# Kernel optimization log

Measured on AMD Instinct MI355X. Metric: run time of the kernel, lower is better.

## Reference

```python
import jax, jax.numpy as jnp
import numpy as np

D = 1024
M = 16
H = D // M  # 64
EPS = 1e-05


def setup_inputs() -> dict:
    key = jax.random.key(0)
    ks = jax.random.split(key, 5)
    B, T = 4, 1024
    x = jax.random.normal(ks[0], (B, T, D), dtype=jnp.float32)
    norm_w = jnp.ones((D,), dtype=jnp.float32)
    s = 1.0 / np.sqrt(D)
    W_v = jax.random.uniform(ks[1], (D, D), dtype=jnp.float32, minval=-s, maxval=s)
    W_a = jax.random.uniform(ks[2], (H * M * (M + 1), D), dtype=jnp.float32, minval=-s, maxval=s)
    W_out = jax.random.uniform(ks[3], (D, D), dtype=jnp.float32, minval=-s, maxval=s)
    return {"x": x, "norm_w": norm_w, "W_v": W_v, "W_a": W_a, "W_out": W_out}


def _rmsnorm(x, w, eps=EPS):
    var = jnp.mean(jnp.square(x), axis=-1, keepdims=True)
    return x * jax.lax.rsqrt(var + eps) * w


def reference(x, norm_w, W_v, W_a, W_out):
    B, T, _ = x.shape
    h = _rmsnorm(x, norm_w)                              # [B,T,D]
    v = (h @ W_v.T).reshape(B, T, H, M)                  # [B,T,H,m]
    gate_logits = (h @ W_a.T).reshape(B, T, H, M, M + 1)
    gates = jax.nn.softmax(gate_logits, axis=-1)
    a0 = gates[..., 0]                                   # [B,T,H,m]
    A = gates[..., 1:]                                   # [B,T,H,m,m]

    # time-major for scan
    A_t = jnp.moveaxis(A, 1, 0)                          # [T,B,H,m,m]
    u_t = jnp.moveaxis(a0 * v, 1, 0)                     # [T,B,H,m]

    def step(state, inp):
        At, ut = inp
        new = jnp.einsum('bhij,bhj->bhi', At, state) + ut
        return new, new

    init = jnp.zeros((B, H, M), dtype=x.dtype)
    _, ys = jax.lax.scan(step, init, (A_t, u_t))         # ys: [T,B,H,m]
    h_out = jnp.moveaxis(ys, 0, 1).reshape(B, T, D)
    return x + h_out @ W_out.T
```

## Files before the change

kernel.cpp:

```cpp
#include <hip/hip_runtime.h>
#include <hip/hip_bf16.h>
#include <math.h>

#define B_DIM 4
#define T_DIM 1024
#define D_DIM 1024
#define M_DIM 16
#define H_DIM 64
#define NT    4096
#define NA    17408
#define NCAT  18432
#define EPSV  1e-5f
#define CL    16
#define NC    64

typedef __bf16 bf16_t;
typedef __bf16 bf16x4 __attribute__((ext_vector_type(4)));
typedef __bf16 bf16x8 __attribute__((ext_vector_type(8)));
typedef float  f32x4  __attribute__((ext_vector_type(4)));

#define PBAR() do { asm volatile("" ::: "memory"); __builtin_amdgcn_s_barrier(); asm volatile("" ::: "memory"); } while (0)

__global__ __launch_bounds__(256) void prep_kernel(const float* __restrict__ x,
                                                   const float* __restrict__ nw,
                                                   const float* __restrict__ Wa,
                                                   const float* __restrict__ Wv,
                                                   const float* __restrict__ Wo,
                                                   bf16_t* __restrict__ h,
                                                   bf16_t* __restrict__ wcat,
                                                   bf16_t* __restrict__ wo) {
  int tid = threadIdx.x;
  if (blockIdx.x < NT) {
    int row = blockIdx.x;
    const float4* xr = reinterpret_cast<const float4*>(x + (size_t)row * D_DIM);
    float4 xv = xr[tid];
    float ss = xv.x * xv.x + xv.y * xv.y + xv.z * xv.z + xv.w * xv.w;
#pragma unroll
    for (int m = 1; m < 64; m <<= 1) ss += __shfl_xor(ss, m, 64);
    __shared__ float red[4];
    int lane = tid & 63, wid = tid >> 6;
    if (lane == 0) red[wid] = ss;
    __syncthreads();
    float tot = red[0] + red[1] + red[2] + red[3];
    float scale = rsqrtf(tot * (1.0f / D_DIM) + EPSV);
    float4 wv = reinterpret_cast<const float4*>(nw)[tid];
    bf16x4 o;
    o[0] = (bf16_t)(xv.x * scale * wv.x);
    o[1] = (bf16_t)(xv.y * scale * wv.y);
    o[2] = (bf16_t)(xv.z * scale * wv.z);
    o[3] = (bf16_t)(xv.w * scale * wv.w);
    reinterpret_cast<bf16x4*>(h)[(size_t)row * 256 + tid] = o;
  } else {
    constexpr int NA4 = NA * D_DIM / 4;
    constexpr int NV4 = D_DIM * D_DIM / 4;
    constexpr int total = NA4 + 2 * NV4;
    int nb = gridDim.x - NT;
    int idx = (blockIdx.x - NT) * 256 + tid;
    int stride = nb * 256;
    for (; idx < total; idx += stride) {
      const float* src; bf16_t* dst; int j;
      if (idx < NA4)            { src = Wa; dst = wcat; j = idx; }
      else if (idx < NA4 + NV4) { src = Wv; dst = wcat + (size_t)NA * D_DIM; j = idx - NA4; }
      else                      { src = Wo; dst = wo; j = idx - NA4 - NV4; }
      float4 v = reinterpret_cast<const float4*>(src)[j];
      bf16x4 o;
      o[0] = (bf16_t)v.x; o[1] = (bf16_t)v.y; o[2] = (bf16_t)v.z; o[3] = (bf16_t)v.w;
      reinterpret_cast<bf16x4*>(dst)[j] = o;
    }
  }
}

__global__ __launch_bounds__(256) void gemm_out_kernel(const bf16_t* __restrict__ A,
                                                       const bf16_t* __restrict__ Bw,
                                                       float* __restrict__ Cout,
                                                       const float* __restrict__ resid,
                                                       int Ndim, int K) {
  constexpr int BM = 128, BN = 128, BK = 32;
  __shared__ bf16_t As[BM * BK];
  __shared__ bf16_t Bs[BN * BK];

  int tid = threadIdx.x;
  int lane = tid & 63;
  int wid = tid >> 6;
  int wm = wid >> 1, wn = wid & 1;
  int bm = blockIdx.x * BM;
  int bn = blockIdx.y * BN;
  int l15 = lane & 15;
  int l4 = lane >> 4;

  f32x4 acc[4][4];
#pragma unroll
  for (int i = 0; i < 4; i++)
#pragma unroll
    for (int j = 0; j < 4; j++) acc[i][j] = (f32x4){0.f, 0.f, 0.f, 0.f};

  const bf16_t* Ag = A + (size_t)bm * K;
  const bf16_t* Bg = Bw + (size_t)bn * K;
  int srow_lane = lane >> 2;
  int scol = (lane & 3) * 8;

  for (int k0 = 0; k0 < K; k0 += BK) {
#pragma unroll
    for (int i = 0; i < 2; i++) {
      int rbase = wid * 32 + i * 16;
      int r = rbase + srow_lane;
      __builtin_amdgcn_global_load_lds(
          (const __attribute__((address_space(1))) void*)(Ag + (size_t)r * K + k0 + scol),
          (__attribute__((address_space(3))) void*)(As + rbase * BK), 16, 0, 0);
      __builtin_amdgcn_global_load_lds(
          (const __attribute__((address_space(1))) void*)(Bg + (size_t)r * K + k0 + scol),
          (__attribute__((address_space(3))) void*)(Bs + rbase * BK), 16, 0, 0);
    }
    __syncthreads();

    const bf16x8* Asv = reinterpret_cast<const bf16x8*>(As);
    const bf16x8* Bsv = reinterpret_cast<const bf16x8*>(Bs);
    bf16x8 af[4], bfr[4];
#pragma unroll
    for (int mf = 0; mf < 4; mf++)
      af[mf] = Asv[(wm * 64 + mf * 16 + l15) * 4 + l4];
#pragma unroll
    for (int nf = 0; nf < 4; nf++)
      bfr[nf] = Bsv[(wn * 64 + nf * 16 + l15) * 4 + l4];
#pragma unroll
    for (int mf = 0; mf < 4; mf++)
#pragma unroll
      for (int nf = 0; nf < 4; nf++)
        acc[mf][nf] = __builtin_amdgcn_mfma_f32_16x16x32_bf16(af[mf], bfr[nf], acc[mf][nf], 0, 0, 0);
    __syncthreads();
  }

#pragma unroll
  for (int mf = 0; mf < 4; mf++)
#pragma unroll
    for (int nf = 0; nf < 4; nf++)
#pragma unroll
      for (int i = 0; i < 4; i++) {
        int row = bm + wm * 64 + mf * 16 + l4 * 4 + i;
        int col = bn + wn * 64 + nf * 16 + l15;
        size_t idx = (size_t)row * Ndim + col;
        Cout[idx] = acc[mf][nf][i] + resid[idx];
      }
}

__global__ __launch_bounds__(512, 2) void gemm256_nt_kernel(const bf16_t* __restrict__ A,
                                                            const bf16_t* __restrict__ Bw,
                                                            bf16_t* __restrict__ Clg,
                                                            float* __restrict__ Cv) {
  constexpr int K = 1024;
  constexpr int G = K / 64;
  __shared__ bf16_t As[2 * 16384];
  __shared__ bf16_t Bs[2 * 16384];

  const int tid = threadIdx.x;
  const int lane = tid & 63;
  const int w = tid >> 6;
  const int wm = w >> 2;
  const int wn = w & 3;
  const int l15 = lane & 15;
  const int l4 = lane >> 4;

  const int bm = blockIdx.x * 256;
  const int bn = blockIdx.y * 256;

  const bf16_t* Ag = A + (size_t)bm * K;
  const bf16_t* Bg = Bw + (size_t)bn * K;

  int growi[2], gcoli[2];
#pragma unroll
  for (int j = 0; j < 2; ++j) {
    int E = j * 4096 + tid * 8;
    int sub = E >> 9, e = E & 511;
    int rin = e >> 5, cs = e & 31;
    int cin = cs ^ ((rin & 8) ? 16 : 0);
    growi[j] = (sub >> 1) * 16 + rin;
    gcoli[j] = (sub & 1) * 32 + cin;
  }

  const int fbase = l15 * 32 + ((l4 * 8) ^ ((l15 & 8) ? 16 : 0));

  f32x4 acc[8][4];
#pragma unroll
  for (int i = 0; i < 8; i++)
#pragma unroll
    for (int j = 0; j < 4; j++) acc[i][j] = (f32x4){0.f, 0.f, 0.f, 0.f};

  bf16x8 ALo[8], AHi[8], B0r[4], B1r[4];

  auto stageHalf = [&](const bf16_t* Gp, bf16_t* Lp, int bufp, int half, int t2) {
#pragma unroll
    for (int j = 0; j < 2; ++j) {
      const bf16_t* src = Gp + (size_t)(half * 128 + growi[j]) * K + t2 * 64 + gcoli[j];
      __builtin_amdgcn_global_load_lds(
          (const __attribute__((address_space(1))) void*)src,
          (__attribute__((address_space(3))) void*)(Lp + bufp * 16384 + half * 8192 + j * 4096 + w * 512),
          16, 0, 0);
    }
  };

  auto rdA4 = [&](bf16x8* dst, int bufp, int rgrpBase) {
    const bf16_t* base = As + bufp * 16384;
#pragma unroll
    for (int mf = 0; mf < 4; ++mf)
#pragma unroll
      for (int kk = 0; kk < 2; ++kk)
        dst[mf * 2 + kk] = *reinterpret_cast<const bf16x8*>(base + ((rgrpBase + mf) * 2 + kk) * 512 + fbase);
  };
  auto rdA2 = [&](bf16x8* dst, int bufp, int rgrpBase) {
    const bf16_t* base = As + bufp * 16384;
#pragma unroll
    for (int mf = 0; mf < 2; ++mf)
#pragma unroll
      for (int kk = 0; kk < 2; ++kk)
        dst[mf * 2 + kk] = *reinterpret_cast<const bf16x8*>(base + ((rgrpBase + mf) * 2 + kk) * 512 + fbase);
  };
  auto rdB = [&](bf16x8* dst, int bufp, int nfBase) {
    const bf16_t* base = Bs + bufp * 16384;
#pragma unroll
    for (int nf = 0; nf < 2; ++nf)
#pragma unroll
      for (int kk = 0; kk < 2; ++kk)
        dst[nf * 2 + kk] = *reinterpret_cast<const bf16x8*>(base + ((wn * 4 + nfBase + nf) * 2 + kk) * 512 + fbase);
  };
  auto MM = [&](const bf16x8* Af, const bf16x8* Bf, int mfB, int nfB) {
    __builtin_amdgcn_s_setprio(1);
#pragma unroll
    for (int mf = 0; mf < 4; ++mf)
#pragma unroll
      for (int nf = 0; nf < 2; ++nf)
#pragma unroll
        for (int kk = 0; kk < 2; ++kk)
          acc[mfB + mf][nfB + nf] = __builtin_amdgcn_mfma_f32_16x16x32_bf16(
              Af[mf * 2 + kk], Bf[nf * 2 + kk], acc[mfB + mf][nfB + nf], 0, 0, 0);
    __builtin_amdgcn_s_setprio(0);
  };

  stageHalf(Bg, Bs, 0, 0, 0);
  stageHalf(Bg, Bs, 0, 1, 0);
  stageHalf(Ag, As, 0, 0, 0);
  stageHalf(Ag, As, 0, 1, 0);
  stageHalf(Ag, As, 1, 0, 1);
  stageHalf(Ag, As, 1, 1, 1);
  asm volatile("s_waitcnt vmcnt(0)" ::: "memory");
  PBAR();
  rdA4(ALo, 0, wm * 8);

#pragma unroll 1
  for (int t = 0; t < G; ++t) {
    const int buf = t & 1;
    const int nbuf = buf ^ 1;

    rdB(B0r, buf, 0);
    rdA2(AHi, buf, wm * 8 + 4);
    if (t + 1 < G) stageHalf(Bg, Bs, nbuf, 0, t + 1);
    PBAR();
    MM(ALo, B0r, 0, 0);
    PBAR();

    rdB(B1r, buf, 2);
    rdA2(AHi + 4, buf, wm * 8 + 6);
    if (t + 1 < G) stageHalf(Bg, Bs, nbuf, 1, t + 1);
    PBAR();
    MM(ALo, B1r, 0, 2);
    if (t + 1 < G) asm volatile("s_waitcnt vmcnt(4)" ::: "memory");
    PBAR();

    if (t + 1 < G) rdA4(ALo, nbuf, wm * 8);
    if (t + 2 < G) stageHalf(Ag, As, buf, 0, t + 2);
    PBAR();
    MM(AHi, B0r, 4, 0);
    PBAR();

    if (t + 2 < G) stageHalf(Ag, As, buf, 1, t + 2);
    PBAR();
    MM(AHi, B1r, 4, 2);
    if (t + 2 < G)      asm volatile("s_waitcnt vmcnt(4)" ::: "memory");
    else if (t + 1 < G) asm volatile("s_waitcnt vmcnt(0)" ::: "memory");
    PBAR();
  }

  if (blockIdx.y < 68) {
#pragma unroll
    for (int mf = 0; mf < 8; ++mf)
#pragma unroll
      for (int nf = 0; nf < 4; ++nf)
#pragma unroll
        for (int i = 0; i < 4; ++i) {
          int row = bm + wm * 128 + mf * 16 + l4 * 4 + i;
          int col = bn + wn * 64 + nf * 16 + l15;
          Clg[(size_t)row * NA + col] = (bf16_t)acc[mf][nf][i];
        }
  } else {
    int cb = bn - NA;
#pragma unroll
    for (int mf = 0; mf < 8; ++mf)
#pragma unroll
      for (int nf = 0; nf < 4; ++nf)
#pragma unroll
        for (int i = 0; i < 4; ++i) {
          int row = bm + wm * 128 + mf * 16 + l4 * 4 + i;
          int col = cb + wn * 64 + nf * 16 + l15;
          Cv[(size_t)row * D_DIM + col] = acc[mf][nf][i];
        }
  }
}

__device__ __forceinline__ void loadLV(const bf16_t* __restrict__ lg,
                                       const float* __restrict__ v,
                                       int r, int h, int i,
                                       ushort* __restrict__ L, float& vv) {
  const ushort* lp = reinterpret_cast<const ushort*>(lg + (size_t)r * NA + h * 272 + i * 17);
#pragma unroll
  for (int j = 0; j < 17; ++j) L[j] = lp[j];
  vv = v[(size_t)r * D_DIM + h * 16 + i];
}

__device__ __forceinline__ void softmax17u(const ushort* __restrict__ L, float vval,
                                           f32x4& a0, f32x4& a1, f32x4& a2, f32x4& a3,
                                           float& u) {
  float e[17];
  float mx = -1e30f;
#pragma unroll
  for (int j = 0; j < 17; ++j) {
    e[j] = __uint_as_float(((unsigned)L[j]) << 16);
    mx = fmaxf(mx, e[j]);
  }
  float s = 0.f;
#pragma unroll
  for (int j = 0; j < 17; ++j) {
    e[j] = __expf(e[j] - mx);
    s += e[j];
  }
  float inv = 1.0f / s;
  a0 = (f32x4){e[1] * inv, e[2] * inv, e[3] * inv, e[4] * inv};
  a1 = (f32x4){e[5] * inv, e[6] * inv, e[7] * inv, e[8] * inv};
  a2 = (f32x4){e[9] * inv, e[10] * inv, e[11] * inv, e[12] * inv};
  a3 = (f32x4){e[13] * inv, e[14] * inv, e[15] * inv, e[16] * inv};
  u = e[0] * inv * vval;
}

__global__ __launch_bounds__(256) void scanA_kernel(const bf16_t* __restrict__ lg,
                                                    const float* __restrict__ v,
                                                    float* __restrict__ sum) {
  int bc = blockIdx.x;
  int b = bc >> 6;
  int c = bc & 63;
  int g = threadIdx.x >> 4;
  int i = threadIdx.x & 15;
  int h = blockIdx.y * 16 + g;
  int chain = b * 64 + h;
  int rbase = b * T_DIM + c * CL;

  __shared__ float Arows[16][16][16];
  __shared__ float Us[16][16];

  f32x4 R0 = (f32x4){i == 0 ? 1.f : 0.f, i == 1 ? 1.f : 0.f, i == 2 ? 1.f : 0.f, i == 3 ? 1.f : 0.f};
  f32x4 R1 = (f32x4){i == 4 ? 1.f : 0.f, i == 5 ? 1.f : 0.f, i == 6 ? 1.f : 0.f, i == 7 ? 1.f : 0.f};
  f32x4 R2 = (f32x4){i == 8 ? 1.f : 0.f, i == 9 ? 1.f : 0.f, i == 10 ? 1.f : 0.f, i == 11 ? 1.f : 0.f};
  f32x4 R3 = (f32x4){i == 12 ? 1.f : 0.f, i == 13 ? 1.f : 0.f, i == 14 ? 1.f : 0.f, i == 15 ? 1.f : 0.f};
  float q = 0.f;

  ushort L[17]; float vv;
  loadLV(lg, v, rbase + CL - 1, h, i, L, vv);

#pragma unroll 1
  for (int tau = CL - 1; tau >= 0; --tau) {
    ushort Ln[17]; float vn;
    int taun = (tau > 0) ? tau - 1 : 0;
    loadLV(lg, v, rbase + taun, h, i, Ln, vn);

    f32x4 a0, a1, a2, a3;
    float uu;
    softmax17u(L, vv, a0, a1, a2, a3, uu);

    *reinterpret_cast<f32x4*>(&Arows[g][i][0]) = a0;
    *reinterpret_cast<f32x4*>(&Arows[g][i][4]) = a1;
    *reinterpret_cast<f32x4*>(&Arows[g][i][8]) = a2;
    *reinterpret_cast<f32x4*>(&Arows[g][i][12]) = a3;
    Us[g][i] = uu;
    asm volatile("s_waitcnt lgkmcnt(0)" ::: "memory");
    __builtin_amdgcn_sched_barrier(0);

    f32x4 u0 = *reinterpret_cast<const f32x4*>(&Us[g][0]);
    f32x4 u1 = *reinterpret_cast<const f32x4*>(&Us[g][4]);
    f32x4 u2 = *reinterpret_cast<const f32x4*>(&Us[g][8]);
    f32x4 u3 = *reinterpret_cast<const f32x4*>(&Us[g][12]);
    float qa = fmaf(R0[0], u0[0], fmaf(R0[1], u0[1], fmaf(R0[2], u0[2], R0[3] * u0[3])));
    float qb = fmaf(R1[0], u1[0], fmaf(R1[1], u1[1], fmaf(R1[2], u1[2], R1[3] * u1[3])));
    float qc = fmaf(R2[0], u2[0], fmaf(R2[1], u2[1], fmaf(R2[2], u2[2], R2[3] * u2[3])));
    float qd = fmaf(R3[0], u3[0], fmaf(R3[1], u3[1], fmaf(R3[2], u3[2], R3[3] * u3[3])));
    q += (qa + qb) + (qc + qd);

    f32x4 n0 = (f32x4){0.f, 0.f, 0.f, 0.f}, n1 = n0, n2 = n0, n3 = n0;
#pragma unroll
    for (int k = 0; k < 16; ++k) {
      float rk = (k < 4) ? R0[k & 3] : (k < 8) ? R1[k & 3] : (k < 12) ? R2[k & 3] : R3[k & 3];
      f32x4 b0 = *reinterpret_cast<const f32x4*>(&Arows[g][k][0]);
      f32x4 b1 = *reinterpret_cast<const f32x4*>(&Arows[g][k][4]);
      f32x4 b2 = *reinterpret_cast<const f32x4*>(&Arows[g][k][8]);
      f32x4 b3 = *reinterpret_cast<const f32x4*>(&Arows[g][k][12]);
#pragma unroll
      for (int e2 = 0; e2 < 4; ++e2) {
        n0[e2] = fmaf(rk, b0[e2], n0[e2]);
        n1[e2] = fmaf(rk, b1[e2], n1[e2]);
        n2[e2] = fmaf(rk, b2[e2], n2[e2]);
        n3[e2] = fmaf(rk, b3[e2], n3[e2]);
      }
    }
    R0 = n0; R1 = n1; R2 = n2; R3 = n3;

#pragma unroll
    for (int j = 0; j < 17; ++j) L[j] = Ln[j];
    vv = vn;
  }

  float* sp = sum + (size_t)(chain * NC + c) * 272;
  *reinterpret_cast<f32x4*>(&sp[i * 16 + 0]) = R0;
  *reinterpret_cast<f32x4*>(&sp[i * 16 + 4]) = R1;
  *reinterpret_cast<f32x4*>(&sp[i * 16 + 8]) = R2;
  *reinterpret_cast<f32x4*>(&sp[i * 16 + 12]) = R3;
  sp[256 + i] = q;
}

__global__ __launch_bounds__(64) void scanB_kernel(const float* __restrict__ sum,
                                                   float* __restrict__ sinit) {
  int chain = blockIdx.x;
  int lane = threadIdx.x;
  int i = lane & 15;

  __shared__ float seg[2][2176];

  const float* gbase = sum + (size_t)chain * NC * 272;

  auto load_seg = [&](int s, int buf) {
#pragma unroll
    for (int r = 0; r < 9; ++r) {
      int idx = r * 256 + lane * 4;
      if (idx < 2176) {
        __builtin_amdgcn_global_load_lds(
            (const __attribute__((address_space(1))) void*)(gbase + (size_t)s * 2176 + idx),
            (__attribute__((address_space(3))) void*)(&seg[buf][r * 256]), 16, 0, 0);
      }
    }
  };

  load_seg(0, 0);
  asm volatile("s_waitcnt vmcnt(0)" ::: "memory");
  __builtin_amdgcn_sched_barrier(0);

  f32x4 S0 = (f32x4){0.f, 0.f, 0.f, 0.f}, S1 = S0, S2 = S0, S3 = S0;
  float own = 0.f;

  for (int sg = 0; sg < 8; ++sg) {
    int buf = sg & 1;
    if (sg + 1 < 8) load_seg(sg + 1, buf ^ 1);
#pragma unroll 1
    for (int cc = 0; cc < 8; ++cc) {
      int c = sg * 8 + cc;
      const float* Pb = &seg[buf][cc * 272];
      if (lane < 16) sinit[(size_t)(chain * NC + c) * 16 + i] = own;

      f32x4 p0 = *reinterpret_cast<const f32x4*>(&Pb[i * 16 + 0]);
      f32x4 p1 = *reinterpret_cast<const f32x4*>(&Pb[i * 16 + 4]);
      f32x4 p2 = *reinterpret_cast<const f32x4*>(&Pb[i * 16 + 8]);
      f32x4 p3 = *reinterpret_cast<const f32x4*>(&Pb[i * 16 + 12]);
      float qq = Pb[256 + i];

      float pa = fmaf(p0[0], S0[0], fmaf(p0[1], S0[1], fmaf(p0[2], S0[2], p0[3] * S0[3])));
      float pb = fmaf(p1[0], S1[0], fmaf(p1[1], S1[1], fmaf(p1[2], S1[2], p1[3] * S1[3])));
      float pc = fmaf(p2[0], S2[0], fmaf(p2[1], S2[1], fmaf(p2[2], S2[2], p2[3] * S2[3])));
      float pd = fmaf(p3[0], S3[0], fmaf(p3[1], S3[1], fmaf(p3[2], S3[2], p3[3] * S3[3])));
      float p = (pa + pb) + (pc + pd) + qq;
      own = p;

#pragma unroll
      for (int j = 0; j < 4; ++j) {
        S0[j] = __shfl(p, j, 64);
        S1[j] = __shfl(p, 4 + j, 64);
        S2[j] = __shfl(p, 8 + j, 64);
        S3[j] = __shfl(p, 12 + j, 64);
      }
    }
    if (sg + 1 < 8) {
      asm volatile("s_waitcnt vmcnt(0)" ::: "memory");
      __builtin_amdgcn_sched_barrier(0);
    }
  }
}

__global__ __launch_bounds__(256) void scanC_kernel(const bf16_t* __restrict__ lg,
                                                    const float* __restrict__ v,
                                                    const float* __restrict__ sinit,
                                                    bf16_t* __restrict__ y) {
  int bc = blockIdx.x;
  int b = bc >> 6;
  int c = bc & 63;
  int g = threadIdx.x >> 4;
  int i = threadIdx.x & 15;
  int h = blockIdx.y * 16 + g;
  int chain = b * 64 + h;
  int rbase = b * T_DIM + c * CL;

  __shared__ float Sb[16][16];

  const float* ip = sinit + (size_t)(chain * NC + c) * 16;
  f32x4 S0 = *reinterpret_cast<const f32x4*>(&ip[0]);
  f32x4 S1 = *reinterpret_cast<const f32x4*>(&ip[4]);
  f32x4 S2 = *reinterpret_cast<const f32x4*>(&ip[8]);
  f32x4 S3 = *reinterpret_cast<const f32x4*>(&ip[12]);

  ushort L[17]; float vv;
  loadLV(lg, v, rbase, h, i, L, vv);

#pragma unroll 1
  for (int t = 0; t < CL; ++t) {
    ushort Ln[17]; float vn;
    int tn = (t < CL - 1) ? t + 1 : t;
    loadLV(lg, v, rbase + tn, h, i, Ln, vn);

    f32x4 a0, a1, a2, a3;
    float uu;
    softmax17u(L, vv, a0, a1, a2, a3, uu);

    float pa = fmaf(a0[0], S0[0], fmaf(a0[1], S0[1], fmaf(a0[2], S0[2], a0[3] * S0[3])));
    float pb = fmaf(a1[0], S1[0], fmaf(a1[1], S1[1], fmaf(a1[2], S1[2], a1[3] * S1[3])));
    float pc = fmaf(a2[0], S2[0], fmaf(a2[1], S2[1], fmaf(a2[2], S2[2], a2[3] * S2[3])));
    float pd = fmaf(a3[0], S3[0], fmaf(a3[1], S3[1], fmaf(a3[2], S3[2], a3[3] * S3[3])));
    float p = (pa + pb) + (pc + pd) + uu;

    y[(size_t)(rbase + t) * D_DIM + h * 16 + i] = (bf16_t)p;

    Sb[g][i] = p;
    asm volatile("s_waitcnt lgkmcnt(0)" ::: "memory");
    __builtin_amdgcn_sched_barrier(0);
    S0 = *reinterpret_cast<const f32x4*>(&Sb[g][0]);
    S1 = *reinterpret_cast<const f32x4*>(&Sb[g][4]);
    S2 = *reinterpret_cast<const f32x4*>(&Sb[g][8]);
    S3 = *reinterpret_cast<const f32x4*>(&Sb[g][12]);

#pragma unroll
    for (int j = 0; j < 17; ++j) L[j] = Ln[j];
    vv = vn;
  }
}

extern "C" void kernel_launch(void* const* d_in, const int* in_sizes, int n_in,
                              void* d_out, int out_size, void* d_ws, size_t ws_size,
                              hipStream_t stream) {
  const float* x      = (const float*)d_in[0];
  const float* norm_w = (const float*)d_in[1];
  const float* W_v    = (const float*)d_in[2];
  const float* W_a    = (const float*)d_in[3];
  const float* W_out  = (const float*)d_in[4];

  char* ws = (char*)d_ws;
  size_t off = 0;
  auto alloc = [&](size_t bytes) {
    void* p = ws + off;
    off += (bytes + 255) & ~(size_t)255;
    return p;
  };
  bf16_t* wcat = (bf16_t*)alloc((size_t)NCAT * D_DIM * 2);
  bf16_t* wo_b = (bf16_t*)alloc((size_t)D_DIM * D_DIM * 2);
  bf16_t* h_b  = (bf16_t*)alloc((size_t)NT * D_DIM * 2);
  float*  v_f  = (float*)alloc((size_t)NT * D_DIM * 4);
  bf16_t* lg_b = (bf16_t*)alloc((size_t)NT * NA * 2);
  bf16_t* y_b  = (bf16_t*)alloc((size_t)NT * D_DIM * 2);
  float*  sum_f   = (float*)alloc((size_t)256 * NC * 272 * 4);
  float*  sinit_f = (float*)alloc((size_t)256 * NC * 16 * 4);

  prep_kernel<<<NT + 2048, 256, 0, stream>>>(x, norm_w, W_a, W_v, W_out,
                                             h_b, wcat, wo_b);

  gemm256_nt_kernel<<<dim3(NT / 256, NCAT / 256), 512, 0, stream>>>(h_b, wcat, lg_b, v_f);

  scanA_kernel<<<dim3(256, 4), 256, 0, stream>>>(lg_b, v_f, sum_f);
  scanB_kernel<<<256, 64, 0, stream>>>(sum_f, sinit_f);
  scanC_kernel<<<dim3(256, 4), 256, 0, stream>>>(lg_b, v_f, sinit_f, y_b);

  gemm_out_kernel<<<dim3(NT / 128, D_DIM / 128), 256, 0, stream>>>(
      y_b, wo_b, (float*)d_out, x, D_DIM, D_DIM);
}
```

Measured before the change: 337.8 us.

## Stage gate logits through LDS with vectorized 16-byte loads in scan kernels

The scan A and C kernels used to load 17 scalar bf16 gate logits per lane with strided 2-byte global loads. They now load each 16-row head block cooperatively with coalesced 16-byte vector loads and stage it in a double-buffered LDS tile. Each lane then reads its 17-element row from LDS. This is meant to cut the number of global load instructions and improve coalescing, at the cost of extra LDS traffic, possible bank conflicts from the stride-17 reads, and explicit vmcnt/lgkmcnt waits.

```diff
diff --git a/kernel.cpp b/kernel.cpp
--- a/kernel.cpp
+++ b/kernel.cpp
@@ -18,8 +18,12 @@
 typedef __bf16 bf16x4 __attribute__((ext_vector_type(4)));
 typedef __bf16 bf16x8 __attribute__((ext_vector_type(8)));
 typedef float  f32x4  __attribute__((ext_vector_type(4)));
+typedef unsigned short u16;
+typedef u16 u16x8 __attribute__((ext_vector_type(8)));
 
 #define PBAR() do { asm volatile("" ::: "memory"); __builtin_amdgcn_s_barrier(); asm volatile("" ::: "memory"); } while (0)
+#define LGKM0() do { asm volatile("s_waitcnt lgkmcnt(0)" ::: "memory"); __builtin_amdgcn_sched_barrier(0); } while (0)
+#define VM0()   do { asm volatile("s_waitcnt vmcnt(0)" ::: "memory"); __builtin_amdgcn_sched_barrier(0); } while (0)
 
 __global__ __launch_bounds__(256) void prep_kernel(const float* __restrict__ x,
                                                    const float* __restrict__ nw,
@@ -305,24 +309,31 @@
   }
 }
 
-__device__ __forceinline__ void loadLV(const bf16_t* __restrict__ lg,
-                                       const float* __restrict__ v,
-                                       int r, int h, int i,
-                                       ushort* __restrict__ L, float& vv) {
-  const ushort* lp = reinterpret_cast<const ushort*>(lg + (size_t)r * NA + h * 272 + i * 17);
-#pragma unroll
-  for (int j = 0; j < 17; ++j) L[j] = lp[j];
-  vv = v[(size_t)r * D_DIM + h * 16 + i];
-}
-
-__device__ __forceinline__ void softmax17u(const ushort* __restrict__ L, float vval,
-                                           f32x4& a0, f32x4& a1, f32x4& a2, f32x4& a3,
-                                           float& u) {
+__device__ __forceinline__ void loadBlk(const bf16_t* __restrict__ lg,
+                                        int r, int h, int i,
+                                        u16x8& c0, u16x8& c1, u16x8& c2) {
+  const u16x8* p = reinterpret_cast<const u16x8*>(lg + (size_t)r * NA + h * 272);
+  c0 = p[i];
+  c1 = p[16 + i];
+  if (i < 2) c2 = p[32 + i];
+}
+
+__device__ __forceinline__ void writeBlk(u16* __restrict__ Lbg, int i,
+                                         const u16x8& c0, const u16x8& c1, const u16x8& c2) {
+  u16x8* q = reinterpret_cast<u16x8*>(Lbg);
+  q[i] = c0;
+  q[16 + i] = c1;
+  if (i < 2) q[32 + i] = c2;
+}
+
+__device__ __forceinline__ void softmax17lds(const u16* __restrict__ Lrow, float vval,
+                                             f32x4& a0, f32x4& a1, f32x4& a2, f32x4& a3,
+                                             float& u) {
   float e[17];
   float mx = -1e30f;
 #pragma unroll
   for (int j = 0; j < 17; ++j) {
-    e[j] = __uint_as_float(((unsigned)L[j]) << 16);
+    e[j] = __uint_as_float(((unsigned)Lrow[j]) << 16);
     mx = fmaxf(mx, e[j]);
   }
   float s = 0.f;
@@ -353,6 +364,7 @@
 
   __shared__ float Arows[16][16][16];
   __shared__ float Us[16][16];
+  __shared__ u16 Lb[2][16][288];
 
   f32x4 R0 = (f32x4){i == 0 ? 1.f : 0.f, i == 1 ? 1.f : 0.f, i == 2 ? 1.f : 0.f, i == 3 ? 1.f : 0.f};
   f32x4 R1 = (f32x4){i == 4 ? 1.f : 0.f, i == 5 ? 1.f : 0.f, i == 6 ? 1.f : 0.f, i == 7 ? 1.f : 0.f};
@@ -360,26 +372,33 @@
   f32x4 R3 = (f32x4){i == 12 ? 1.f : 0.f, i == 13 ? 1.f : 0.f, i == 14 ? 1.f : 0.f, i == 15 ? 1.f : 0.f};
   float q = 0.f;
 
-  ushort L[17]; float vv;
-  loadLV(lg, v, rbase + CL - 1, h, i, L, vv);
+  {
+    u16x8 c0, c1, c2;
+    loadBlk(lg, rbase + CL - 1, h, i, c0, c1, c2);
+    VM0();
+    writeBlk(&Lb[0][g][0], i, c0, c1, c2);
+  }
+  float vv = v[(size_t)(rbase + CL - 1) * D_DIM + h * 16 + i];
+  int cur = 0;
 
 #pragma unroll 1
   for (int tau = CL - 1; tau >= 0; --tau) {
-    ushort Ln[17]; float vn;
     int taun = (tau > 0) ? tau - 1 : 0;
-    loadLV(lg, v, rbase + taun, h, i, Ln, vn);
-
+    u16x8 n0, n1, n2;
+    loadBlk(lg, rbase + taun, h, i, n0, n1, n2);
+    float vn = v[(size_t)(rbase + taun) * D_DIM + h * 16 + i];
+
+    LGKM0();
     f32x4 a0, a1, a2, a3;
     float uu;
-    softmax17u(L, vv, a0, a1, a2, a3, uu);
+    softmax17lds(&Lb[cur][g][i * 17], vv, a0, a1, a2, a3, uu);
 
     *reinterpret_cast<f32x4*>(&Arows[g][i][0]) = a0;
     *reinterpret_cast<f32x4*>(&Arows[g][i][4]) = a1;
     *reinterpret_cast<f32x4*>(&Arows[g][i][8]) = a2;
     *reinterpret_cast<f32x4*>(&Arows[g][i][12]) = a3;
     Us[g][i] = uu;
-    asm volatile("s_waitcnt lgkmcnt(0)" ::: "memory");
-    __builtin_amdgcn_sched_barrier(0);
+    LGKM0();
 
     f32x4 u0 = *reinterpret_cast<const f32x4*>(&Us[g][0]);
     f32x4 u1 = *reinterpret_cast<const f32x4*>(&Us[g][4]);
@@ -391,7 +410,7 @@
     float qd = fmaf(R3[0], u3[0], fmaf(R3[1], u3[1], fmaf(R3[2], u3[2], R3[3] * u3[3])));
     q += (qa + qb) + (qc + qd);
 
-    f32x4 n0 = (f32x4){0.f, 0.f, 0.f, 0.f}, n1 = n0, n2 = n0, n3 = n0;
+    f32x4 m0 = (f32x4){0.f, 0.f, 0.f, 0.f}, m1 = m0, m2 = m0, m3 = m0;
 #pragma unroll
     for (int k = 0; k < 16; ++k) {
       float rk = (k < 4) ? R0[k & 3] : (k < 8) ? R1[k & 3] : (k < 12) ? R2[k & 3] : R3[k & 3];
@@ -401,17 +420,18 @@
       f32x4 b3 = *reinterpret_cast<const f32x4*>(&Arows[g][k][12]);
 #pragma unroll
       for (int e2 = 0; e2 < 4; ++e2) {
-        n0[e2] = fmaf(rk, b0[e2], n0[e2]);
-        n1[e2] = fmaf(rk, b1[e2], n1[e2]);
-        n2[e2] = fmaf(rk, b2[e2], n2[e2]);
-        n3[e2] = fmaf(rk, b3[e2], n3[e2]);
+        m0[e2] = fmaf(rk, b0[e2], m0[e2]);
+        m1[e2] = fmaf(rk, b1[e2], m1[e2]);
+        m2[e2] = fmaf(rk, b2[e2], m2[e2]);
+        m3[e2] = fmaf(rk, b3[e2], m3[e2]);
       }
     }
-    R0 = n0; R1 = n1; R2 = n2; R3 = n3;
-
-#pragma unroll
-    for (int j = 0; j < 17; ++j) L[j] = Ln[j];
+    R0 = m0; R1 = m1; R2 = m2; R3 = m3;
+
+    VM0();
+    writeBlk(&Lb[cur ^ 1][g][0], i, n0, n1, n2);
     vv = vn;
+    cur ^= 1;
   }
 
   float* sp = sum + (size_t)(chain * NC + c) * 272;
@@ -445,8 +465,7 @@
   };
 
   load_seg(0, 0);
-  asm volatile("s_waitcnt vmcnt(0)" ::: "memory");
-  __builtin_amdgcn_sched_barrier(0);
+  VM0();
 
   f32x4 S0 = (f32x4){0.f, 0.f, 0.f, 0.f}, S1 = S0, S2 = S0, S3 = S0;
   float own = 0.f;
@@ -481,10 +500,7 @@
         S3[j] = __shfl(p, 12 + j, 64);
       }
     }
-    if (sg + 1 < 8) {
-      asm volatile("s_waitcnt vmcnt(0)" ::: "memory");
-      __builtin_amdgcn_sched_barrier(0);
-    }
+    if (sg + 1 < 8) VM0();
   }
 }
 
@@ -502,6 +518,7 @@
   int rbase = b * T_DIM + c * CL;
 
   __shared__ float Sb[16][16];
+  __shared__ u16 Lb[2][16][288];
 
   const float* ip = sinit + (size_t)(chain * NC + c) * 16;
   f32x4 S0 = *reinterpret_cast<const f32x4*>(&ip[0]);
@@ -509,18 +526,26 @@
   f32x4 S2 = *reinterpret_cast<const f32x4*>(&ip[8]);
   f32x4 S3 = *reinterpret_cast<const f32x4*>(&ip[12]);
 
-  ushort L[17]; float vv;
-  loadLV(lg, v, rbase, h, i, L, vv);
+  {
+    u16x8 c0, c1, c2;
+    loadBlk(lg, rbase, h, i, c0, c1, c2);
+    VM0();
+    writeBlk(&Lb[0][g][0], i, c0, c1, c2);
+  }
+  float vv = v[(size_t)rbase * D_DIM + h * 16 + i];
+  int cur = 0;
 
 #pragma unroll 1
   for (int t = 0; t < CL; ++t) {
-    ushort Ln[17]; float vn;
     int tn = (t < CL - 1) ? t + 1 : t;
-    loadLV(lg, v, rbase + tn, h, i, Ln, vn);
-
+    u16x8 n0, n1, n2;
+    loadBlk(lg, rbase + tn, h, i, n0, n1, n2);
+    float vn = v[(size_t)(rbase + tn) * D_DIM + h * 16 + i];
+
+    LGKM0();
     f32x4 a0, a1, a2, a3;
     float uu;
-    softmax17u(L, vv, a0, a1, a2, a3, uu);
+    softmax17lds(&Lb[cur][g][i * 17], vv, a0, a1, a2, a3, uu);
 
     float pa = fmaf(a0[0], S0[0], fmaf(a0[1], S0[1], fmaf(a0[2], S0[2], a0[3] * S0[3])));
     float pb = fmaf(a1[0], S1[0], fmaf(a1[1], S1[1], fmaf(a1[2], S1[2], a1[3] * S1[3])));
@@ -531,16 +556,16 @@
     y[(size_t)(rbase + t) * D_DIM + h * 16 + i] = (bf16_t)p;
 
     Sb[g][i] = p;
-    asm volatile("s_waitcnt lgkmcnt(0)" ::: "memory");
-    __builtin_amdgcn_sched_barrier(0);
+    LGKM0();
     S0 = *reinterpret_cast<const f32x4*>(&Sb[g][0]);
     S1 = *reinterpret_cast<const f32x4*>(&Sb[g][4]);
     S2 = *reinterpret_cast<const f32x4*>(&Sb[g][8]);
     S3 = *reinterpret_cast<const f32x4*>(&Sb[g][12]);
 
-#pragma unroll
-    for (int j = 0; j < 17; ++j) L[j] = Ln[j];
+    VM0();
+    writeBlk(&Lb[cur ^ 1][g][0], i, n0, n1, n2);
     vv = vn;
+    cur ^= 1;
   }
 }
 
```

After: 372.5 us. +10.3%, slower.
